# Kernel optimization log

Hardware: AMD Instinct MI355X
Metric: run time of the kernel (lower is better)

Reference implementation:

```python
import jax, jax.numpy as jnp
import numpy as np

N, E, G = 50000, 800000, 512          # nodes, edges, graphs in batch
DIN, DH, H, DOUT = 128, 128, 2, 128   # dim_in, dim_h, heads, dim_out
NEG_SLOPE = 0.2
EPS_BN = 1e-5


def setup_inputs():
    key = jax.random.key(0)
    ks = jax.random.split(key, 12)
    def glorot(k, shape, fan):
        return (jax.random.normal(k, shape, jnp.float32) / np.float32(np.sqrt(fan)))
    return dict(
        x=jax.random.normal(ks[0], (N, DIN), jnp.float32),
        edge_index=jax.random.randint(ks[1], (2, E), 0, N, dtype=jnp.int32),
        batch=jnp.sort(jax.random.randint(ks[2], (N,), 0, G, dtype=jnp.int32)),
        Wl1=glorot(ks[3], (DIN, H * DH), DIN),
        Wr1=glorot(ks[4], (DIN, H * DH), DIN),
        att1=glorot(ks[5], (H, DH), DH),
        b1=jnp.zeros((H * DH,), jnp.float32),
        gamma=jnp.ones((H * DH,), jnp.float32),
        beta=jnp.zeros((H * DH,), jnp.float32),
        Wl2=glorot(ks[6], (H * DH, DOUT), H * DH),
        Wr2=glorot(ks[7], (H * DH, DOUT), H * DH),
        att2=glorot(ks[8], (1, DOUT), DOUT),
        b2=jnp.zeros((DOUT,), jnp.float32),
        Wlin=glorot(ks[9], (DOUT, 2), DOUT),
        blin=jnp.zeros((2,), jnp.float32),
    )


def gatv2_conv(x, src, dst, Wl, Wr, att, bias, heads, dh, n):
    # x: [n, F]; src/dst: [Etot] (self-loops already appended)
    xl = (x @ Wl).reshape(n, heads, dh)  # source transform (messages)
    xr = (x @ Wr).reshape(n, heads, dh)  # target transform
    m = xl[src] + xr[dst]                             # [Etot, H, dh]
    e = jnp.einsum('ehd,hd->eh', jax.nn.leaky_relu(m, NEG_SLOPE), att)  # [Etot, H]
    # softmax over incoming edges of each target node
    emax = jax.ops.segment_max(e, dst, num_segments=n)
    ex = jnp.exp(e - emax[dst])
    denom = jax.ops.segment_sum(ex, dst, num_segments=n)
    alpha = ex / (denom[dst] + 1e-16)                 # [Etot, H]
    out = jax.ops.segment_sum(xl[src] * alpha[:, :, None], dst, num_segments=n)
    return out.reshape(n, heads * dh) + bias


def reference(x, edge_index, batch, Wl1, Wr1, att1, b1, gamma, beta,
              Wl2, Wr2, att2, b2, Wlin, blin):
    loops = jnp.arange(N, dtype=edge_index.dtype)
    src = jnp.concatenate([edge_index[0], loops])
    dst = jnp.concatenate([edge_index[1], loops])

    h = gatv2_conv(x, src, dst, Wl1, Wr1, att1, b1, H, DH, N)   # [N, H*DH]
    h = jax.nn.elu(h)
    # BatchNorm over node dimension (training-mode batch stats)
    mu = h.mean(axis=0)
    var = h.var(axis=0)
    h = (h - mu) * jax.lax.rsqrt(var + EPS_BN) * gamma + beta
    # dropout p=0 -> identity
    h = gatv2_conv(h, src, dst, Wl2, Wr2, att2, b2, 1, DOUT, N)  # [N, DOUT]

    # global mean pool per graph
    s = jax.ops.segment_sum(h, batch, num_segments=G)
    cnt = jax.ops.segment_sum(jnp.ones((N,), h.dtype), batch, num_segments=G)
    pooled = s / jnp.maximum(cnt, 1.0)[:, None]                  # [G, DOUT]
    return pooled @ Wlin + blin                                  # [G, 2]
```

## Files before the change

### kernel.cpp

```cpp
#include <hip/hip_runtime.h>


#define DIN 128
#define F1 256
#define F2 128
#define NEG_SLOPE 0.2f

typedef unsigned short u16;
typedef __attribute__((ext_vector_type(8))) short short8;
typedef __attribute__((ext_vector_type(4))) float floatx4;

__device__ __forceinline__ float bf2f(u16 u) {
  return __uint_as_float(((unsigned int)u) << 16);
}
__device__ __forceinline__ u16 f2bf(float f) {
  unsigned int x = __float_as_uint(f);
  return (u16)((x + 0x7fffu + ((x >> 16) & 1u)) >> 16);
}
__device__ __forceinline__ void load8(const u16* p, float (&f)[8]) {
  short8 v = *(const short8*)p;
#pragma unroll
  for (int k = 0; k < 8; k++) f[k] = bf2f((u16)v[k]);
}

struct PTab { const void* src[8]; int off[9]; };
__global__ __launch_bounds__(256) void k_convert_all(
    const void* __restrict__ xsrc, u16* __restrict__ xb, int n4, int nxb,
    PTab t, u16* __restrict__ pb, int ptotal, int npb,
    const void* __restrict__ Wl1s, const void* __restrict__ Wr1s,
    const void* __restrict__ Wl2s, const void* __restrict__ Wr2s,
    u16* __restrict__ Wl1t, u16* __restrict__ Wr1t,
    u16* __restrict__ Wl2t, u16* __restrict__ Wr2t, int* __restrict__ flag) {
  __shared__ int flagS;
  int tid = threadIdx.x;
  if (tid < 64) {
    int cnt = 0;
#pragma unroll
    for (int i = 0; i < 2; ++i) {
      u16 v = ((const u16*)xsrc)[2 * (tid + 64 * i)];
      int e = (v >> 7) & 0xFF;
      if (e >= 115 && e <= 130) cnt++;
    }
#pragma unroll
    for (int m = 1; m <= 32; m <<= 1) cnt += __shfl_xor(cnt, m, 64);
    if (tid == 0) flagS = (cnt < 64) ? 1 : 0;
  }
  __syncthreads();
  const int fl = flagS;
  if (blockIdx.x == 0 && tid == 0) *flag = fl;

  int b = blockIdx.x;
  if (b < nxb) {
    int i = b * 256 + tid;
    if (i >= n4) return;
    if (fl) {
      float4 a = ((const float4*)xsrc)[i];
      ushort4 o;
      o.x = f2bf(a.x); o.y = f2bf(a.y); o.z = f2bf(a.z); o.w = f2bf(a.w);
      ((ushort4*)xb)[i] = o;
    } else {
      ((ulong1*)xb)[i] = ((const ulong1*)xsrc)[i];
    }
    return;
  }
  b -= nxb;
  if (b < npb) {
    int i = b * 256 + tid;
    if (i >= ptotal) return;
    int s = 0;
#pragma unroll
    for (int k = 1; k < 8; k++) s += (i >= t.off[k]);
    int local = i - t.off[s];
    pb[i] = fl ? f2bf(((const float*)t.src[s])[local]) : ((const u16*)t.src[s])[local];
    return;
  }
  b -= npb;
  int seg = b >> 7;
  int i = (b & 127) * 256 + tid;
  const void* s; u16* d; int NL, sh;
  if      (seg == 0) { s = Wl1s; d = Wl1t; NL = 256; sh = 7; }
  else if (seg == 1) { s = Wr1s; d = Wr1t; NL = 256; sh = 7; }
  else if (seg == 2) { s = Wl2s; d = Wl2t; NL = 128; sh = 8; }
  else               { s = Wr2s; d = Wr2t; NL = 128; sh = 8; }
  int n = i >> sh, k = i & ((1 << sh) - 1);
  int si = k * NL + n;
  d[i] = fl ? f2bf(((const float*)s)[si]) : ((const u16*)s)[si];
}

__global__ void k_hist(const int* __restrict__ ei, int* __restrict__ hist,
                       const int* __restrict__ batch, int* __restrict__ gcnt,
                       int E, int Etot, int N) {
  int e = blockIdx.x * 256 + threadIdx.x;
  if (e >= Etot) return;
  int dst = (e < E) ? ei[E + e] : (e - E);
  atomicAdd(&hist[dst], 1);
  if (e < N) atomicAdd(&gcnt[batch[e]], 1);
}

__global__ void k_scan1(const int* __restrict__ in, int* __restrict__ out,
                        int* __restrict__ partials, int n) {
  __shared__ int tmp[256];
  int t = threadIdx.x;
  int gid = blockIdx.x * 256 + t;
  int v = (gid < n) ? in[gid] : 0;
  tmp[t] = v;
  __syncthreads();
  for (int off = 1; off < 256; off <<= 1) {
    int add = (t >= off) ? tmp[t - off] : 0;
    __syncthreads();
    tmp[t] += add;
    __syncthreads();
  }
  if (gid < n) out[gid] = tmp[t] - v;
  if (t == 255) partials[blockIdx.x] = tmp[255];
}

__global__ void k_scan2(int* __restrict__ partials, int nb) {
  __shared__ int tmp[256];
  __shared__ int carry_s;
  int t = threadIdx.x;
  if (t == 0) carry_s = 0;
  __syncthreads();
  for (int base = 0; base < nb; base += 256) {
    int idx = base + t;
    int v = (idx < nb) ? partials[idx] : 0;
    tmp[t] = v;
    __syncthreads();
    for (int off = 1; off < 256; off <<= 1) {
      int add = (t >= off) ? tmp[t - off] : 0;
      __syncthreads();
      tmp[t] += add;
      __syncthreads();
    }
    int carry = carry_s;
    if (idx < nb) partials[idx] = tmp[t] - v + carry;
    __syncthreads();
    if (t == 255) carry_s = carry + tmp[255];
    __syncthreads();
  }
}

__global__ void k_scan3(int* __restrict__ rowptr, const int* __restrict__ partials,
                        int* __restrict__ cursor, int n, int Etot) {
  int gid = blockIdx.x * 256 + threadIdx.x;
  if (gid < n) {
    int v = rowptr[gid] + partials[blockIdx.x];
    rowptr[gid] = v;
    cursor[gid] = v;
  }
  if (gid == 0) rowptr[n] = Etot;
}

__global__ void k_scatter(const int* __restrict__ ei, int* __restrict__ cursor,
                          int* __restrict__ ssrc, int E, int Etot) {
  int e = blockIdx.x * 256 + threadIdx.x;
  if (e >= Etot) return;
  int src, dst;
  if (e < E) { src = ei[e]; dst = ei[E + e]; }
  else       { src = e - E; dst = e - E; }
  int pos = atomicAdd(&cursor[dst], 1);
  ssrc[pos] = src;
}

template<int K, bool RB>
__global__ __launch_bounds__(256) void k_gemm(
    const u16* __restrict__ A, const u16* __restrict__ Blt, const u16* __restrict__ Brt,
    int NL, u16* __restrict__ Cl, u16* __restrict__ Cr, int M,
    const float* __restrict__ rbias) {
  const int tid = threadIdx.x;
  const int m0 = blockIdx.x * 64;
  const int n0g = blockIdx.y * 64;
  const u16* Bt; u16* C; int col0;
  if (n0g < NL) { Bt = Blt; C = Cl; col0 = n0g; }
  else          { Bt = Brt; C = Cr; col0 = n0g - NL; }

  const int wave = tid >> 6, lane = tid & 63;
  const int wm = wave >> 1, wn = wave & 1;
  const int quad = lane >> 4, l16 = lane & 15;

  floatx4 acc[2][2] = {};
#pragma unroll
  for (int k0 = 0; k0 < K; k0 += 32) {
    short8 af[2], bfr[2];
#pragma unroll
    for (int mt = 0; mt < 2; mt++) {
      int row = m0 + wm * 32 + mt * 16 + l16;
      if (row > M - 1) row = M - 1;
      af[mt] = *(const short8*)(A + (size_t)row * K + k0 + quad * 8);
    }
#pragma unroll
    for (int nt = 0; nt < 2; nt++) {
      int nn = col0 + wn * 32 + nt * 16 + l16;
      bfr[nt] = *(const short8*)(Bt + (size_t)nn * K + k0 + quad * 8);
    }
#pragma unroll
    for (int mt = 0; mt < 2; mt++)
#pragma unroll
      for (int nt = 0; nt < 2; nt++)
        acc[mt][nt] = __builtin_amdgcn_mfma_f32_16x16x32_bf16(af[mt], bfr[nt], acc[mt][nt], 0, 0, 0);
  }

#pragma unroll
  for (int mt = 0; mt < 2; mt++)
#pragma unroll
    for (int nt = 0; nt < 2; nt++) {
      float rb = 0.f;
      if (RB) rb = rbias[n0g + wn * 32 + nt * 16 + l16];
#pragma unroll
      for (int r = 0; r < 4; r++) {
        int row = m0 + wm * 32 + mt * 16 + quad * 4 + r;
        if (row < M) {
          int col = col0 + wn * 32 + nt * 16 + l16;
          C[(size_t)row * NL + col] = f2bf(acc[mt][nt][r] + rb);
        }
      }
    }
}

template<int HEADS, int MODE>
__global__ __launch_bounds__(256) void k_agg(
    const u16* __restrict__ xl, const u16* __restrict__ xr,
    const u16* __restrict__ att, const u16* __restrict__ bias,
    const int* __restrict__ rowptr, const int* __restrict__ ssrc,
    void* __restrict__ outv, int n) {
  constexpr int F = HEADS * 128;
  constexpr int EPI = 4 / HEADS;
  int wave = threadIdx.x >> 6, lane = threadIdx.x & 63;
  int node = blockIdx.x * 4 + wave;
  if (node >= n) return;
  const int q = lane >> 4, l = lane & 15;
  const int eo   = (HEADS == 2) ? (q >> 1) : q;
  const int head = (HEADS == 2) ? (q & 1) : 0;
  const int ch0 = head * 128 + l * 8;

  float xrv[8], attv[8], acc[8];
  load8(xr + (size_t)node * F + ch0, xrv);
  load8(att + ch0, attv);
#pragma unroll
  for (int k = 0; k < 8; k++) acc[k] = 0.f;

  float l_run = 0.f;
  const int jb = rowptr[node], je = rowptr[node + 1];
  for (int j = jb; j < je; j += EPI) {
    int jj = j + eo;
    int src = ssrc[jj < je ? jj : (je - 1)];
    float xlv[8];
    load8(xl + (size_t)src * F + ch0, xlv);
    float s = 0.f;
#pragma unroll
    for (int k = 0; k < 8; k++) {
      float mm = xlv[k] + xrv[k];
      mm = mm > 0.f ? mm : NEG_SLOPE * mm;
      s += mm * attv[k];
    }
#pragma unroll
    for (int m = 1; m <= 8; m <<= 1) s += __shfl_xor(s, m, 64);
    float p = (jj < je) ? __expf(fminf(s, 80.f)) : 0.f;
    l_run += p;
#pragma unroll
    for (int k = 0; k < 8; k++) acc[k] += p * xlv[k];
  }

#pragma unroll
  for (int m = 16 * HEADS; m <= 32; m <<= 1) {
#pragma unroll
    for (int k = 0; k < 8; k++) acc[k] += __shfl_xor(acc[k], m, 64);
    l_run += __shfl_xor(l_run, m, 64);
  }

  if (lane < 16 * HEADS) {
    float inv = 1.f / (l_run + 1e-16f);
    if (MODE == 0) {
      short8 o;
#pragma unroll
      for (int k = 0; k < 8; k++) {
        float t = acc[k] * inv + bf2f(bias[ch0 + k]);
        t = t > 0.f ? t : (__expf(t) - 1.f);
        o[k] = (short)f2bf(t);
      }
      *(short8*)((u16*)outv + (size_t)node * F + ch0) = o;
    } else {
      float v[8];
#pragma unroll
      for (int k = 0; k < 8; k++) v[k] = acc[k] * inv + bf2f(bias[ch0 + k]);
      float* op = (float*)outv + (size_t)node * F + ch0;
      *(float4*)op = make_float4(v[0], v[1], v[2], v[3]);
      *(float4*)(op + 4) = make_float4(v[4], v[5], v[6], v[7]);
    }
  }
}

__global__ void k_stats(const u16* __restrict__ h, float* __restrict__ gsum,
                        float* __restrict__ gsumsq, int n) {
  int c = threadIdx.x;
  int r0 = blockIdx.x * 256;
  int r1 = min(r0 + 256, n);
  float s = 0.f, ss = 0.f;
  for (int r = r0; r < r1; ++r) {
    float v = bf2f(h[(size_t)r * F1 + c]);
    s += v; ss += v * v;
  }
  atomicAdd(&gsum[c], s);
  atomicAdd(&gsumsq[c], ss);
}

__global__ __launch_bounds__(256) void k_foldbn(
    const float* __restrict__ gsum, const float* __restrict__ gsumsq,
    const u16* __restrict__ gamma, const u16* __restrict__ beta,
    u16* __restrict__ Wl2t, u16* __restrict__ Wr2t,
    float* __restrict__ rbias, float invn) {
  __shared__ float red[8];
  int t = threadIdx.x, n = blockIdx.x;
  float mu = gsum[t] * invn;
  float var = gsumsq[t] * invn - mu * mu;
  float a = bf2f(gamma[t]) * rsqrtf(fmaxf(var, 0.f) + 1e-5f);
  float b = bf2f(beta[t]) - mu * a;
  float wl = bf2f(Wl2t[n * 256 + t]);
  float wr = bf2f(Wr2t[n * 256 + t]);
  float sl = b * wl, sr = b * wr;
  Wl2t[n * 256 + t] = f2bf(a * wl);
  Wr2t[n * 256 + t] = f2bf(a * wr);
#pragma unroll
  for (int m = 1; m <= 32; m <<= 1) {
    sl += __shfl_xor(sl, m, 64);
    sr += __shfl_xor(sr, m, 64);
  }
  int wave = t >> 6, lane = t & 63;
  if (lane == 0) { red[wave] = sl; red[4 + wave] = sr; }
  __syncthreads();
  if (t == 0) rbias[n] = red[0] + red[1] + red[2] + red[3];
  if (t == 1) rbias[128 + n] = red[4] + red[5] + red[6] + red[7];
}

__global__ __launch_bounds__(256) void k_poolfinal(
    const float* __restrict__ h2, const int* __restrict__ grptr,
    const u16* __restrict__ Wlin, const u16* __restrict__ blin,
    void* __restrict__ out, const int* __restrict__ flag, int G, int N) {
  __shared__ float sm[4][128];
  int g = blockIdx.x;
  int wave = threadIdx.x >> 6, lane = threadIdx.x & 63;
  int jb = grptr[g];
  int je = (g == G - 1) ? N : grptr[g + 1];
  int ch = lane * 2;
  float c0 = 0.f, c1 = 0.f;
  for (int r = jb + wave; r < je; r += 4) {
    float2 v = *(const float2*)(h2 + (size_t)r * F2 + ch);
    c0 += v.x; c1 += v.y;
  }
  sm[wave][ch] = c0;
  sm[wave][ch + 1] = c1;
  __syncthreads();
  if (wave == 0) {
    c0 = sm[0][ch] + sm[1][ch] + sm[2][ch] + sm[3][ch];
    c1 = sm[0][ch + 1] + sm[1][ch + 1] + sm[2][ch + 1] + sm[3][ch + 1];
    float cf = fmaxf((float)(je - jb), 1.f);
    c0 /= cf; c1 /= cf;
    float s0 = c0 * bf2f(Wlin[ch * 2 + 0]) + c1 * bf2f(Wlin[(ch + 1) * 2 + 0]);
    float s1 = c0 * bf2f(Wlin[ch * 2 + 1]) + c1 * bf2f(Wlin[(ch + 1) * 2 + 1]);
#pragma unroll
    for (int m = 1; m <= 32; m <<= 1) {
      s0 += __shfl_xor(s0, m, 64);
      s1 += __shfl_xor(s1, m, 64);
    }
    if (lane == 0) {
      float o0 = s0 + bf2f(blin[0]);
      float o1 = s1 + bf2f(blin[1]);
      if (*flag) {
        ((float*)out)[g * 2 + 0] = o0;
        ((float*)out)[g * 2 + 1] = o1;
      } else {
        ((u16*)out)[g * 2 + 0] = f2bf(o0);
        ((u16*)out)[g * 2 + 1] = f2bf(o1);
      }
    }
  }
}

extern "C" void kernel_launch(void* const* d_in, const int* in_sizes, int n_in,
                              void* d_out, int out_size, void* d_ws, size_t ws_size,
                              hipStream_t stream) {
  const int* ei    = (const int*)d_in[1];
  const int* batch = (const int*)d_in[2];

  const int N = in_sizes[0] / DIN;
  const int E = in_sizes[1] / 2;
  const int G = out_size / 2;
  const int Etot = E + N;

  char* p = (char*)d_ws;
  auto alloc = [&](size_t bytes) {
    char* r = p;
    p += (bytes + 255) & ~(size_t)255;
    return r;
  };
  int*  flag     = (int*)alloc(256);
  int*  hist     = (int*)alloc((size_t)N * 4);
  float* gsum    = (float*)alloc((size_t)F1 * 4);
  float* gsumsq  = (float*)alloc((size_t)F1 * 4);
  int*  gcnt     = (int*)alloc((size_t)G * 4);
  size_t zero_span = (size_t)((char*)gcnt + (size_t)G * 4 - (char*)hist);
  int*  rowptr   = (int*)alloc((size_t)(N + 1) * 4);
  int*  cursor   = (int*)alloc((size_t)N * 4);
  int*  partials = (int*)alloc(4096);
  float* rbias   = (float*)alloc(256 * 4);
  int*  ssrc     = (int*)alloc((size_t)Etot * 4);
  u16*  xb       = (u16*)alloc((size_t)N * DIN * 2);
  u16*  pb       = (u16*)alloc(4096);
  u16*  Wl1t     = (u16*)alloc(DIN * F1 * 2);
  u16*  Wr1t     = (u16*)alloc(DIN * F1 * 2);
  u16*  Wl2t     = (u16*)alloc(F1 * F2 * 2);
  u16*  Wr2t     = (u16*)alloc(F1 * F2 * 2);
  u16*  regionA  = (u16*)alloc((size_t)N * F1 * 2);
  u16*  regionB  = (u16*)alloc((size_t)N * F1 * 2);
  u16*  regionC  = (u16*)alloc((size_t)N * F1 * 2);

  u16*  xl1  = regionA;
  u16*  xr1  = regionB;
  u16*  helu = regionC;
  u16*  xl2  = regionB;
  u16*  xr2  = regionB + (size_t)N * F2;
  float* h2  = (float*)regionA;

  const int pidx[8] = {5, 6, 7, 8, 11, 12, 13, 14};
  PTab tab;
  int accum = 0;
  for (int i = 0; i < 8; i++) {
    tab.src[i] = d_in[pidx[i]];
    tab.off[i] = accum;
    accum += in_sizes[pidx[i]];
  }
  tab.off[8] = accum;
  int n4 = in_sizes[0] / 4;
  int nxb = (n4 + 255) / 256;
  int npb = (accum + 255) / 256;
  k_convert_all<<<nxb + npb + 512, 256, 0, stream>>>(
      d_in[0], xb, n4, nxb, tab, pb, accum, npb,
      d_in[3], d_in[4], d_in[9], d_in[10], Wl1t, Wr1t, Wl2t, Wr2t, flag);
  u16 *pAtt1 = pb + tab.off[0], *pB1 = pb + tab.off[1], *pGamma = pb + tab.off[2],
      *pBeta = pb + tab.off[3], *pAtt2 = pb + tab.off[4], *pB2 = pb + tab.off[5],
      *pWlin = pb + tab.off[6], *pBlin = pb + tab.off[7];

  hipMemsetAsync(hist, 0, zero_span, stream);

  const int eb = (Etot + 255) / 256;
  const int sb = (N + 255) / 256;

  k_hist<<<eb, 256, 0, stream>>>(ei, hist, batch, gcnt, E, Etot, N);
  k_scan1<<<sb, 256, 0, stream>>>(hist, rowptr, partials, N);
  k_scan2<<<1, 256, 0, stream>>>(partials, sb);
  k_scan3<<<sb, 256, 0, stream>>>(rowptr, partials, cursor, N, Etot);
  k_scatter<<<eb, 256, 0, stream>>>(ei, cursor, ssrc, E, Etot);

  dim3 g1((N + 63) / 64, (2 * F1) / 64);
  k_gemm<DIN, false><<<g1, 256, 0, stream>>>(xb, Wl1t, Wr1t, F1, xl1, xr1, N, nullptr);

  k_agg<2, 0><<<(N + 3) / 4, 256, 0, stream>>>(xl1, xr1, pAtt1, pB1, rowptr, ssrc, helu, N);

  k_stats<<<sb, 256, 0, stream>>>(helu, gsum, gsumsq, N);
  k_foldbn<<<128, 256, 0, stream>>>(gsum, gsumsq, pGamma, pBeta, Wl2t, Wr2t, rbias,
                                    1.0f / (float)N);

  dim3 g2((N + 63) / 64, (2 * F2) / 64);
  k_gemm<F1, true><<<g2, 256, 0, stream>>>(helu, Wl2t, Wr2t, F2, xl2, xr2, N, rbias);

  k_agg<1, 1><<<(N + 3) / 4, 256, 0, stream>>>(xl2, xr2, pAtt2, pB2, rowptr, ssrc, h2, N);

  k_scan2<<<1, 256, 0, stream>>>(gcnt, G);
  k_poolfinal<<<G, 256, 0, stream>>>(h2, gcnt, pWlin, pBlin, d_out, flag, G, N);
}
```

Measured before the change: 539.0 us.

## Cut launches: single-pass decoupled scan, fused zeroing, binary-search pooling, vectorized stats

Replaces the three-kernel prefix scan with a single-pass decoupled-lookback scan that uses an atomic block counter. The memset is folded into the convert kernel, and the per-graph count histogram plus its scan are replaced by binary searches over the sorted batch array inside the pooling kernel. BatchNorm statistics now use a grid-stride kernel with vectorized 8-wide loads and a shared-memory reduction, cutting the number of global atomics. The goal is fewer kernel launches and less serial work. The cost is reliance on spin-wait forward progress in the scan and on the batch array being sorted.

```diff
diff --git a/kernel.cpp b/kernel.cpp
--- a/kernel.cpp
+++ b/kernel.cpp
@@ -30,7 +30,8 @@
     const void* __restrict__ Wl1s, const void* __restrict__ Wr1s,
     const void* __restrict__ Wl2s, const void* __restrict__ Wr2s,
     u16* __restrict__ Wl1t, u16* __restrict__ Wr1t,
-    u16* __restrict__ Wl2t, u16* __restrict__ Wr2t, int* __restrict__ flag) {
+    u16* __restrict__ Wl2t, u16* __restrict__ Wr2t,
+    int* __restrict__ zbase, int zn, int* __restrict__ flag) {
   __shared__ int flagS;
   int tid = threadIdx.x;
   if (tid < 64) {
@@ -75,34 +76,43 @@
     return;
   }
   b -= npb;
-  int seg = b >> 7;
-  int i = (b & 127) * 256 + tid;
-  const void* s; u16* d; int NL, sh;
-  if      (seg == 0) { s = Wl1s; d = Wl1t; NL = 256; sh = 7; }
-  else if (seg == 1) { s = Wr1s; d = Wr1t; NL = 256; sh = 7; }
-  else if (seg == 2) { s = Wl2s; d = Wl2t; NL = 128; sh = 8; }
-  else               { s = Wr2s; d = Wr2t; NL = 128; sh = 8; }
-  int n = i >> sh, k = i & ((1 << sh) - 1);
-  int si = k * NL + n;
-  d[i] = fl ? f2bf(((const float*)s)[si]) : ((const u16*)s)[si];
+  if (b < 512) {
+    int seg = b >> 7;
+    int i = (b & 127) * 256 + tid;
+    const void* s; u16* d; int NL, sh;
+    if      (seg == 0) { s = Wl1s; d = Wl1t; NL = 256; sh = 7; }
+    else if (seg == 1) { s = Wr1s; d = Wr1t; NL = 256; sh = 7; }
+    else if (seg == 2) { s = Wl2s; d = Wl2t; NL = 128; sh = 8; }
+    else               { s = Wr2s; d = Wr2t; NL = 128; sh = 8; }
+    int n = i >> sh, k = i & ((1 << sh) - 1);
+    int si = k * NL + n;
+    d[i] = fl ? f2bf(((const float*)s)[si]) : ((const u16*)s)[si];
+    return;
+  }
+  b -= 512;
+  int i = b * 256 + tid;
+  if (i < zn) zbase[i] = 0;
 }
 
 __global__ void k_hist(const int* __restrict__ ei, int* __restrict__ hist,
-                       const int* __restrict__ batch, int* __restrict__ gcnt,
-                       int E, int Etot, int N) {
+                       int E, int Etot) {
   int e = blockIdx.x * 256 + threadIdx.x;
   if (e >= Etot) return;
   int dst = (e < E) ? ei[E + e] : (e - E);
   atomicAdd(&hist[dst], 1);
-  if (e < N) atomicAdd(&gcnt[batch[e]], 1);
-}
-
-__global__ void k_scan1(const int* __restrict__ in, int* __restrict__ out,
-                        int* __restrict__ partials, int n) {
+}
+
+__global__ void k_scan(const int* __restrict__ hist, int* __restrict__ rowptr,
+                       int* __restrict__ cursor, unsigned long long* __restrict__ pstate,
+                       int* __restrict__ ctr, int n, int Etot) {
   __shared__ int tmp[256];
+  __shared__ int bidS, offS;
   int t = threadIdx.x;
-  int gid = blockIdx.x * 256 + t;
-  int v = (gid < n) ? in[gid] : 0;
+  if (t == 0) bidS = atomicAdd(ctr, 1);
+  __syncthreads();
+  int bid = bidS;
+  int gid = bid * 256 + t;
+  int v = (gid < n) ? hist[gid] : 0;
   tmp[t] = v;
   __syncthreads();
   for (int off = 1; off < 256; off <<= 1) {
@@ -111,42 +121,32 @@
     tmp[t] += add;
     __syncthreads();
   }
-  if (gid < n) out[gid] = tmp[t] - v;
-  if (t == 255) partials[blockIdx.x] = tmp[255];
-}
-
-__global__ void k_scan2(int* __restrict__ partials, int nb) {
-  __shared__ int tmp[256];
-  __shared__ int carry_s;
-  int t = threadIdx.x;
-  if (t == 0) carry_s = 0;
-  __syncthreads();
-  for (int base = 0; base < nb; base += 256) {
-    int idx = base + t;
-    int v = (idx < nb) ? partials[idx] : 0;
-    tmp[t] = v;
-    __syncthreads();
-    for (int off = 1; off < 256; off <<= 1) {
-      int add = (t >= off) ? tmp[t - off] : 0;
-      __syncthreads();
-      tmp[t] += add;
-      __syncthreads();
-    }
-    int carry = carry_s;
-    if (idx < nb) partials[idx] = tmp[t] - v + carry;
-    __syncthreads();
-    if (t == 255) carry_s = carry + tmp[255];
-    __syncthreads();
-  }
-}
-
-__global__ void k_scan3(int* __restrict__ rowptr, const int* __restrict__ partials,
-                        int* __restrict__ cursor, int n, int Etot) {
-  int gid = blockIdx.x * 256 + threadIdx.x;
+  if (t == 0) {
+    int total = tmp[255];
+    unsigned long long st =
+        ((unsigned long long)(bid == 0 ? 2 : 1) << 32) | (unsigned)total;
+    atomicExch(&pstate[bid], st);
+    int off = 0;
+    if (bid > 0) {
+      int b = bid - 1;
+      while (true) {
+        unsigned long long s;
+        do { s = atomicAdd(&pstate[b], 0ULL); } while ((s >> 32) == 0);
+        off += (int)(unsigned)s;
+        if ((s >> 32) == 2) break;
+        b--;
+      }
+      atomicExch(&pstate[bid],
+                 ((unsigned long long)2 << 32) | (unsigned)(off + total));
+    }
+    offS = off;
+  }
+  __syncthreads();
+  int off = offS;
   if (gid < n) {
-    int v = rowptr[gid] + partials[blockIdx.x];
-    rowptr[gid] = v;
-    cursor[gid] = v;
+    int ex = off + tmp[t] - v;
+    rowptr[gid] = ex;
+    cursor[gid] = ex;
   }
   if (gid == 0) rowptr[n] = Etot;
 }
@@ -290,18 +290,28 @@
   }
 }
 
-__global__ void k_stats(const u16* __restrict__ h, float* __restrict__ gsum,
-                        float* __restrict__ gsumsq, int n) {
-  int c = threadIdx.x;
-  int r0 = blockIdx.x * 256;
-  int r1 = min(r0 + 256, n);
-  float s = 0.f, ss = 0.f;
-  for (int r = r0; r < r1; ++r) {
-    float v = bf2f(h[(size_t)r * F1 + c]);
-    s += v; ss += v * v;
-  }
-  atomicAdd(&gsum[c], s);
-  atomicAdd(&gsumsq[c], ss);
+__global__ __launch_bounds__(256) void k_stats(
+    const u16* __restrict__ h, float* __restrict__ gsum,
+    float* __restrict__ gsumsq, int n) {
+  __shared__ float smS[8][256], smQ[8][256];
+  int t = threadIdx.x;
+  int rg = t >> 5, cl = t & 31;
+  int ch0 = cl * 8;
+  float s[8] = {}, q[8] = {};
+  for (int r = blockIdx.x * 8 + rg; r < n; r += gridDim.x * 8) {
+    float v[8];
+    load8(h + (size_t)r * F1 + ch0, v);
+#pragma unroll
+    for (int k = 0; k < 8; k++) { s[k] += v[k]; q[k] += v[k] * v[k]; }
+  }
+#pragma unroll
+  for (int k = 0; k < 8; k++) { smS[rg][ch0 + k] = s[k]; smQ[rg][ch0 + k] = q[k]; }
+  __syncthreads();
+  float ts = 0.f, tq = 0.f;
+#pragma unroll
+  for (int g = 0; g < 8; g++) { ts += smS[g][t]; tq += smQ[g][t]; }
+  atomicAdd(&gsum[t], ts);
+  atomicAdd(&gsumsq[t], tq);
 }
 
 __global__ __launch_bounds__(256) void k_foldbn(
@@ -332,15 +342,21 @@
   if (t == 1) rbias[128 + n] = red[4] + red[5] + red[6] + red[7];
 }
 
+__device__ __forceinline__ int lowerb(const int* __restrict__ a, int n, int key) {
+  int lo = 0, hi = n;
+  while (lo < hi) { int m = (lo + hi) >> 1; if (a[m] < key) lo = m + 1; else hi = m; }
+  return lo;
+}
+
 __global__ __launch_bounds__(256) void k_poolfinal(
-    const float* __restrict__ h2, const int* __restrict__ grptr,
+    const float* __restrict__ h2, const int* __restrict__ batch,
     const u16* __restrict__ Wlin, const u16* __restrict__ blin,
     void* __restrict__ out, const int* __restrict__ flag, int G, int N) {
   __shared__ float sm[4][128];
   int g = blockIdx.x;
   int wave = threadIdx.x >> 6, lane = threadIdx.x & 63;
-  int jb = grptr[g];
-  int je = (g == G - 1) ? N : grptr[g + 1];
+  int jb = lowerb(batch, N, g);
+  int je = lowerb(batch, N, g + 1);
   int ch = lane * 2;
   float c0 = 0.f, c1 = 0.f;
   for (int r = jb + wave; r < je; r += 4) {
@@ -395,13 +411,13 @@
   };
   int*  flag     = (int*)alloc(256);
   int*  hist     = (int*)alloc((size_t)N * 4);
-  float* gsum    = (float*)alloc((size_t)F1 * 4);
-  float* gsumsq  = (float*)alloc((size_t)F1 * 4);
-  int*  gcnt     = (int*)alloc((size_t)G * 4);
-  size_t zero_span = (size_t)((char*)gcnt + (size_t)G * 4 - (char*)hist);
+  float* gsum    = (float*)alloc(1024);
+  float* gsumsq  = (float*)alloc(1024);
+  unsigned long long* pstate = (unsigned long long*)alloc(2048);
+  int*  ctr      = (int*)alloc(256);
+  int   zn       = (int)(((char*)ctr + 256) - (char*)hist) / 4;
   int*  rowptr   = (int*)alloc((size_t)(N + 1) * 4);
   int*  cursor   = (int*)alloc((size_t)N * 4);
-  int*  partials = (int*)alloc(4096);
   float* rbias   = (float*)alloc(256 * 4);
   int*  ssrc     = (int*)alloc((size_t)Etot * 4);
   u16*  xb       = (u16*)alloc((size_t)N * DIN * 2);
@@ -433,22 +449,20 @@
   int n4 = in_sizes[0] / 4;
   int nxb = (n4 + 255) / 256;
   int npb = (accum + 255) / 256;
-  k_convert_all<<<nxb + npb + 512, 256, 0, stream>>>(
+  int nzb = (zn + 255) / 256;
+  k_convert_all<<<nxb + npb + 512 + nzb, 256, 0, stream>>>(
       d_in[0], xb, n4, nxb, tab, pb, accum, npb,
-      d_in[3], d_in[4], d_in[9], d_in[10], Wl1t, Wr1t, Wl2t, Wr2t, flag);
+      d_in[3], d_in[4], d_in[9], d_in[10], Wl1t, Wr1t, Wl2t, Wr2t,
+      hist, zn, flag);
   u16 *pAtt1 = pb + tab.off[0], *pB1 = pb + tab.off[1], *pGamma = pb + tab.off[2],
       *pBeta = pb + tab.off[3], *pAtt2 = pb + tab.off[4], *pB2 = pb + tab.off[5],
       *pWlin = pb + tab.off[6], *pBlin = pb + tab.off[7];
 
-  hipMemsetAsync(hist, 0, zero_span, stream);
-
   const int eb = (Etot + 255) / 256;
   const int sb = (N + 255) / 256;
 
-  k_hist<<<eb, 256, 0, stream>>>(ei, hist, batch, gcnt, E, Etot, N);
-  k_scan1<<<sb, 256, 0, stream>>>(hist, rowptr, partials, N);
-  k_scan2<<<1, 256, 0, stream>>>(partials, sb);
-  k_scan3<<<sb, 256, 0, stream>>>(rowptr, partials, cursor, N, Etot);
+  k_hist<<<eb, 256, 0, stream>>>(ei, hist, E, Etot);
+  k_scan<<<sb, 256, 0, stream>>>(hist, rowptr, cursor, pstate, ctr, N, Etot);
   k_scatter<<<eb, 256, 0, stream>>>(ei, cursor, ssrc, E, Etot);
 
   dim3 g1((N + 63) / 64, (2 * F1) / 64);
@@ -456,7 +470,7 @@
 
   k_agg<2, 0><<<(N + 3) / 4, 256, 0, stream>>>(xl1, xr1, pAtt1, pB1, rowptr, ssrc, helu, N);
 
-  k_stats<<<sb, 256, 0, stream>>>(helu, gsum, gsumsq, N);
+  k_stats<<<256, 256, 0, stream>>>(helu, gsum, gsumsq, N);
   k_foldbn<<<128, 256, 0, stream>>>(gsum, gsumsq, pGamma, pBeta, Wl2t, Wr2t, rbias,
                                     1.0f / (float)N);
 
@@ -465,6 +479,5 @@
 
   k_agg<1, 1><<<(N + 3) / 4, 256, 0, stream>>>(xl2, xr2, pAtt2, pB2, rowptr, ssrc, h2, N);
 
-  k_scan2<<<1, 256, 0, stream>>>(gcnt, G);
-  k_poolfinal<<<G, 256, 0, stream>>>(h2, gcnt, pWlin, pBlin, d_out, flag, G, N);
-}
+  k_poolfinal<<<G, 256, 0, stream>>>(h2, batch, pWlin, pBlin, d_out, flag, G, N);
+}
```

New measurement: 455.2 us. 1.18x faster.
